# Kernel tuning notes

Measured on AMD Instinct MI355X. Metric: run time of the kernel, lower is better.

The kernel has to match this reference:

```python
import jax, jax.numpy as jnp
import numpy as np

B, N, K, H = 2, 2048, 48, 128
NIN = 2 * H          # num_in = 2*num_hidden (ProteinMPNN wiring)
FF = 4 * H           # PositionWiseFeedForward hidden
SCALE = 30.0
EPS = 1e-5           # torch LayerNorm default eps


def _ln(x, g, b):
    m = jnp.mean(x, axis=-1, keepdims=True)
    v = jnp.mean((x - m) ** 2, axis=-1, keepdims=True)
    return (x - m) / jnp.sqrt(v + EPS) * g + b


def _gelu(x):
    return jax.nn.gelu(x, approximate=False)  # torch.nn.GELU default (erf)


def _lin(x, W, b):
    return x @ W + b


def setup_inputs() -> dict:
    key = jax.random.key(0)
    ks = jax.random.split(key, 24)
    s = 0.05
    inp = {
        "h_V": jax.random.normal(ks[0], (B, N, H), jnp.float32),
        "h_E": jax.random.normal(ks[1], (B, N, K, H), jnp.float32),
        "E_idx": jax.random.randint(ks[2], (B, N, K), 0, N, jnp.int64),
        "mask_V": jnp.ones((B, N), jnp.float32),
        "mask_attend": jnp.ones((B, N, K), jnp.float32),
        # message MLP (node update): W1 in = H + NIN = 3H
        "W1": jax.random.normal(ks[3], (3 * H, H), jnp.float32) * s,
        "b1": jnp.zeros((H,), jnp.float32),
        "W2": jax.random.normal(ks[4], (H, H), jnp.float32) * s,
        "b2": jnp.zeros((H,), jnp.float32),
        "W3": jax.random.normal(ks[5], (H, H), jnp.float32) * s,
        "b3": jnp.zeros((H,), jnp.float32),
        # PositionWiseFeedForward
        "Wd_in": jax.random.normal(ks[6], (H, FF), jnp.float32) * s,
        "bd_in": jnp.zeros((FF,), jnp.float32),
        "Wd_out": jax.random.normal(ks[7], (FF, H), jnp.float32) * s,
        "bd_out": jnp.zeros((H,), jnp.float32),
        # edge-update MLP: W11 in = H + NIN = 3H
        "W11": jax.random.normal(ks[8], (3 * H, H), jnp.float32) * s,
        "b11": jnp.zeros((H,), jnp.float32),
        "W12": jax.random.normal(ks[9], (H, H), jnp.float32) * s,
        "b12": jnp.zeros((H,), jnp.float32),
        "W13": jax.random.normal(ks[10], (H, H), jnp.float32) * s,
        "b13": jnp.zeros((H,), jnp.float32),
        # LayerNorms
        "n1g": jnp.ones((H,), jnp.float32), "n1b": jnp.zeros((H,), jnp.float32),
        "n2g": jnp.ones((H,), jnp.float32), "n2b": jnp.zeros((H,), jnp.float32),
        "n3g": jnp.ones((H,), jnp.float32), "n3b": jnp.zeros((H,), jnp.float32),
    }
    return inp


def reference(h_V, h_E, E_idx, mask_V, mask_attend,
              W1, b1, W2, b2, W3, b3,
              Wd_in, bd_in, Wd_out, bd_out,
              W11, b11, W12, b12, W13, b13,
              n1g, n1b, n2g, n2b, n3g, n3b):
    gather = jax.vmap(lambda hv, idx: hv[idx])  # [B,N,H],[B,N,K] -> [B,N,K,H]

    # --- node update: cat_neighbors_nodes + expand + 3-layer GELU MLP ---
    h_nb = gather(h_V, E_idx)                                   # [B,N,K,H]
    hV_exp = jnp.broadcast_to(h_V[:, :, None, :], h_nb.shape)   # [B,N,K,H]
    h_EV = jnp.concatenate([hV_exp, h_E, h_nb], axis=-1)        # [B,N,K,3H]
    h_msg = _lin(_gelu(_lin(_gelu(_lin(h_EV, W1, b1)), W2, b2)), W3, b3)
    h_msg = mask_attend[..., None] * h_msg
    dh = jnp.sum(h_msg, axis=-2) / SCALE                        # masked-sum reduce
    h_V = _ln(h_V + dh, n1g, n1b)

    # --- position-wise FFN ---
    dh = _lin(_gelu(_lin(h_V, Wd_in, bd_in)), Wd_out, bd_out)
    h_V = _ln(h_V + dh, n2g, n2b)
    h_V = mask_V[..., None] * h_V

    # --- edge update (not last layer) ---
    h_nb2 = gather(h_V, E_idx)
    hV_exp2 = jnp.broadcast_to(h_V[:, :, None, :], h_nb2.shape)
    h_EV2 = jnp.concatenate([hV_exp2, h_E, h_nb2], axis=-1)     # [B,N,K,3H]
    h_msg2 = _lin(_gelu(_lin(_gelu(_lin(h_EV2, W11, b11)), W12, b12)), W13, b13)
    h_E = _ln(h_E + h_msg2, n3g, n3b)
    return (h_V, h_E)
```

## Files before the change

kernel.cpp:

```cpp
#include <hip/hip_runtime.h>
#include <stdint.h>

#define XP2 264
#define MP 136
#define EPIP 132
#define FFP 520

typedef __attribute__((ext_vector_type(8))) short bf16x8;
typedef __attribute__((ext_vector_type(4))) float f32x4;

__device__ __forceinline__ f32x4 mfma16(bf16x8 a, bf16x8 b, f32x4 c) {
  return __builtin_amdgcn_mfma_f32_16x16x32_bf16(a, b, c, 0, 0, 0);
}

__device__ __forceinline__ uint16_t f2b(float f) {
  union { float f; uint32_t u; } v; v.f = f;
  uint32_t u = v.u;
  uint32_t r = u + 0x7fffu + ((u >> 16) & 1u);
  return (uint16_t)(r >> 16);
}
__device__ __forceinline__ uint32_t pk2(float a, float b) {
  return (uint32_t)f2b(a) | ((uint32_t)f2b(b) << 16);
}
__device__ __forceinline__ float gelu_f(float x) {
  float z = 0.7978845608028654f * (x + 0.044715f * x * x * x);
  float e = __expf(2.0f * z);
  float t = 1.0f - 2.0f / (e + 1.0f);
  return 0.5f * x * (1.0f + t);
}

__global__ __launch_bounds__(256) void k_prep(
    const float* __restrict__ hV,
    const float* __restrict__ W1, const float* __restrict__ W2, const float* __restrict__ W3,
    const float* __restrict__ WdIn, const float* __restrict__ WdOut,
    const float* __restrict__ W11, const float* __restrict__ W12, const float* __restrict__ W13,
    uint16_t* __restrict__ hVb,
    uint16_t* __restrict__ W1t, uint16_t* __restrict__ W2t, uint16_t* __restrict__ W3t,
    uint16_t* __restrict__ WdInT, uint16_t* __restrict__ WdOutT,
    uint16_t* __restrict__ W11t, uint16_t* __restrict__ W12t, uint16_t* __restrict__ W13t) {
  int i = blockIdx.x * 256 + threadIdx.x;
  if (i < 524288) { hVb[i] = f2b(hV[i]); return; }
  int j = i - 524288;
  if (j < 49152) { int n = j / 384, k = j - n * 384; W1t[j] = f2b(W1[k * 128 + n]); return; }
  j -= 49152;
  if (j < 16384) { int n = j >> 7, k = j & 127; W2t[j] = f2b(W2[k * 128 + n]); return; }
  j -= 16384;
  if (j < 16384) { int n = j >> 7, k = j & 127; W3t[j] = f2b(W3[k * 128 + n]); return; }
  j -= 16384;
  if (j < 65536) { int n = j >> 7, k = j & 127; WdInT[j] = f2b(WdIn[k * 512 + n]); return; }
  j -= 65536;
  if (j < 65536) { int n = j >> 9, k = j & 511; WdOutT[j] = f2b(WdOut[k * 128 + n]); return; }
  j -= 65536;
  if (j < 49152) { int n = j / 384, k = j - n * 384; W11t[j] = f2b(W11[k * 128 + n]); return; }
  j -= 49152;
  if (j < 16384) { int n = j >> 7, k = j & 127; W12t[j] = f2b(W12[k * 128 + n]); return; }
  j -= 16384;
  if (j < 16384) { int n = j >> 7, k = j & 127; W13t[j] = f2b(W13[k * 128 + n]); return; }
}

__global__ __launch_bounds__(256) void k_vec(
    const uint16_t* __restrict__ Xb, const uint16_t* __restrict__ Wt,
    float* __restrict__ C) {
  const int tid = threadIdx.x;
  const int lane = tid & 63, w = tid >> 6, l15 = lane & 15, lg = lane >> 4;
  const int row0 = blockIdx.x * 64 + w * 16;
  f32x4 acc[8] = {};
#pragma unroll
  for (int ks = 0; ks < 4; ++ks) {
    bf16x8 a = *(const bf16x8*)(Xb + (row0 + l15) * 128 + ks * 32 + lg * 8);
#pragma unroll
    for (int j = 0; j < 8; ++j) {
      bf16x8 bb = *(const bf16x8*)(Wt + (j * 16 + l15) * 384 + ks * 32 + lg * 8);
      acc[j] = mfma16(a, bb, acc[j]);
    }
  }
#pragma unroll
  for (int j = 0; j < 8; ++j)
#pragma unroll
    for (int r = 0; r < 4; ++r)
      C[(row0 + lg * 4 + r) * 128 + j * 16 + l15] = acc[j][r];
}

#define BUILD_XT(GSRC)                                                              \
  do {                                                                              \
    for (int idx = tid; idx < 48 * 32; idx += 256) {                                \
      int k_ = idx >> 5;                                                            \
      int c_ = idx & 31;                                                            \
      uint4 v_;                                                                     \
      if (c_ < 16) {                                                                \
        const float* s_ = hE + (size_t)(bn * 48 + k_) * 128 + (c_ << 3);            \
        float4 f0_ = *(const float4*)s_;                                            \
        float4 f1_ = *(const float4*)(s_ + 4);                                      \
        v_ = make_uint4(pk2(f0_.x, f0_.y), pk2(f0_.z, f0_.w),                       \
                        pk2(f1_.x, f1_.y), pk2(f1_.z, f1_.w));                      \
      } else {                                                                      \
        v_ = *(const uint4*)((GSRC) + nbr[k_] * 128 + ((c_ - 16) << 3));            \
      }                                                                             \
      *(uint4*)(xt + k_ * XP2 + (c_ << 3)) = v_;                                    \
    }                                                                               \
  } while (0)

#define LAYER256(WT, ACC)                                                           \
  do {                                                                              \
    const uint16_t* wr0_ = (WT) + (w * 32 + l15) * 384 + 128 + lg * 8;              \
    const uint16_t* wr1_ = (WT) + (w * 32 + 16 + l15) * 384 + 128 + lg * 8;         \
    _Pragma("unroll 2") for (int ks = 0; ks < 8; ++ks) {                            \
      bf16x8 bA_ = *(const bf16x8*)(wr0_ + ks * 32);                                \
      bf16x8 bB_ = *(const bf16x8*)(wr1_ + ks * 32);                                \
      _Pragma("unroll") for (int m = 0; m < 3; ++m) {                               \
        bf16x8 a_ = *(const bf16x8*)(xt + (m * 16 + l15) * XP2 + ks * 32 + lg * 8); \
        ACC[m][0] = mfma16(a_, bA_, ACC[m][0]);                                     \
        ACC[m][1] = mfma16(a_, bB_, ACC[m][1]);                                     \
      }                                                                             \
    }                                                                               \
  } while (0)

#define LAYER128(WT, ASRC, ACC)                                                     \
  do {                                                                              \
    const uint16_t* wr0_ = (WT) + (w * 32 + l15) * 128 + lg * 8;                    \
    const uint16_t* wr1_ = (WT) + (w * 32 + 16 + l15) * 128 + lg * 8;               \
    _Pragma("unroll") for (int ks = 0; ks < 4; ++ks) {                              \
      bf16x8 bA_ = *(const bf16x8*)(wr0_ + ks * 32);                                \
      bf16x8 bB_ = *(const bf16x8*)(wr1_ + ks * 32);                                \
      _Pragma("unroll") for (int m = 0; m < 3; ++m) {                               \
        bf16x8 a_ = *(const bf16x8*)((ASRC) + (m * 16 + l15) * MP + ks * 32 + lg * 8); \
        ACC[m][0] = mfma16(a_, bA_, ACC[m][0]);                                     \
        ACC[m][1] = mfma16(a_, bB_, ACC[m][1]);                                     \
      }                                                                              \
    }                                                                               \
  } while (0)

#define GSTORE(ACC, BIAS, DST)                                                      \
  do {                                                                              \
    float bA_ = (BIAS)[w * 32 + l15];                                               \
    float bB_ = (BIAS)[w * 32 + 16 + l15];                                          \
    _Pragma("unroll") for (int m = 0; m < 3; ++m)                                   \
    _Pragma("unroll") for (int r = 0; r < 4; ++r) {                                 \
      int row_ = m * 16 + lg * 4 + r;                                               \
      (DST)[row_ * MP + w * 32 + l15] = f2b(gelu_f(ACC[m][0][r] + bA_));            \
      (DST)[row_ * MP + w * 32 + 16 + l15] = f2b(gelu_f(ACC[m][1][r] + bB_));       \
    }                                                                               \
  } while (0)

#define ACC_INIT(ACC, CV)                                                           \
  do {                                                                              \
    float c0_ = (CV)[bn * 128 + w * 32 + l15];                                      \
    float c1_ = (CV)[bn * 128 + w * 32 + 16 + l15];                                 \
    _Pragma("unroll") for (int m = 0; m < 3; ++m) {                                 \
      ACC[m][0] = (f32x4){c0_, c0_, c0_, c0_};                                      \
      ACC[m][1] = (f32x4){c1_, c1_, c1_, c1_};                                      \
    }                                                                               \
  } while (0)

__global__ __launch_bounds__(256, 4) void k_node(
    const float* __restrict__ hV, const float* __restrict__ hE,
    const int* __restrict__ eidx, const float* __restrict__ maskA,
    const float* __restrict__ bias1, const float* __restrict__ bias2,
    const float* __restrict__ bias3,
    const float* __restrict__ g1, const float* __restrict__ be1,
    const uint16_t* __restrict__ hVb, const float* __restrict__ C1,
    const uint16_t* __restrict__ W1t, const uint16_t* __restrict__ W2t,
    const uint16_t* __restrict__ W3t,
    float* __restrict__ hV1, uint16_t* __restrict__ hV1b) {
  __shared__ __align__(16) unsigned char lds[39296];
  uint16_t* xt = (uint16_t*)lds;
  uint16_t* midA = (uint16_t*)(lds + 25344);
  uint16_t* midB = (uint16_t*)lds;
  float* dh = (float*)(lds + 38400);
  int* nbr = (int*)(lds + 38912);
  float* amask = (float*)(lds + 39104);

  const int tid = threadIdx.x;
  const int lane = tid & 63;
  const int w = tid >> 6;
  const int l15 = lane & 15;
  const int lg = lane >> 4;
  const int bn = blockIdx.x;
  const int b = bn >> 11;

  if (tid < 48) {
    nbr[tid] = (b << 11) + eidx[bn * 48 + tid];
    amask[tid] = maskA[bn * 48 + tid];
  }
  __syncthreads();

  BUILD_XT(hVb);
  __syncthreads();

  f32x4 acc1[3][2];
  ACC_INIT(acc1, C1);
  LAYER256(W1t, acc1);
  GSTORE(acc1, bias1, midA);
  __syncthreads();

  f32x4 acc2[3][2] = {};
  LAYER128(W2t, midA, acc2);
  GSTORE(acc2, bias2, midB);
  __syncthreads();

  f32x4 acc3[3][2] = {};
  LAYER128(W3t, midB, acc3);

  {
    float bA = bias3[w * 32 + l15];
    float bB = bias3[w * 32 + 16 + l15];
    float s0 = 0.f, s1 = 0.f;
#pragma unroll
    for (int m = 0; m < 3; ++m)
#pragma unroll
      for (int r = 0; r < 4; ++r) {
        int row = m * 16 + lg * 4 + r;
        float mk = amask[row];
        s0 += (acc3[m][0][r] + bA) * mk;
        s1 += (acc3[m][1][r] + bB) * mk;
      }
    s0 += __shfl_xor(s0, 16); s0 += __shfl_xor(s0, 32);
    s1 += __shfl_xor(s1, 16); s1 += __shfl_xor(s1, 32);
    if (lg == 0) { dh[w * 32 + l15] = s0; dh[w * 32 + 16 + l15] = s1; }
  }
  __syncthreads();

  if (w == 0) {
    const float inv = 1.0f / 30.0f;
    float x0 = hV[bn * 128 + lane] + dh[lane] * inv;
    float x1 = hV[bn * 128 + 64 + lane] + dh[64 + lane] * inv;
    float s = x0 + x1, q = x0 * x0 + x1 * x1;
#pragma unroll
    for (int off = 1; off < 64; off <<= 1) {
      s += __shfl_xor(s, off);
      q += __shfl_xor(q, off);
    }
    float mean = s * (1.0f / 128.0f);
    float var = q * (1.0f / 128.0f) - mean * mean;
    float rstd = rsqrtf(var + 1e-5f);
    float y0 = (x0 - mean) * rstd * g1[lane] + be1[lane];
    float y1 = (x1 - mean) * rstd * g1[64 + lane] + be1[64 + lane];
    hV1[bn * 128 + lane] = y0;
    hV1[bn * 128 + 64 + lane] = y1;
    hV1b[bn * 128 + lane] = f2b(y0);
    hV1b[bn * 128 + 64 + lane] = f2b(y1);
  }
}

__global__ __launch_bounds__(256, 2) void k_ffn(
    const float* __restrict__ hV1, const uint16_t* __restrict__ hV1b,
    const float* __restrict__ maskV,
    const float* __restrict__ bdin, const float* __restrict__ bdout,
    const float* __restrict__ g2, const float* __restrict__ be2,
    const uint16_t* __restrict__ WdInT, const uint16_t* __restrict__ WdOutT,
    float* __restrict__ outV, uint16_t* __restrict__ hV2b) {
  __shared__ __align__(16) unsigned char lds[20992];
  uint16_t* xa = (uint16_t*)lds;
  uint16_t* mf = (uint16_t*)(lds + 4352);
  float* epi = (float*)(lds + 4352);

  const int tid = threadIdx.x;
  const int lane = tid & 63;
  const int w = tid >> 6;
  const int l15 = lane & 15;
  const int lg = lane >> 4;
  const int node0 = blockIdx.x * 16;

  {
    int row = tid >> 4, c = tid & 15;
    *(uint4*)(xa + row * 136 + (c << 3)) =
        *(const uint4*)(hV1b + (node0 + row) * 128 + (c << 3));
  }
  __syncthreads();

  f32x4 acc[8] = {};
  {
    const uint16_t* ar = xa + l15 * 136 + lg * 8;
#pragma unroll
    for (int ks = 0; ks < 4; ++ks) {
      bf16x8 a = *(const bf16x8*)(ar + ks * 32);
#pragma unroll
      for (int j = 0; j < 8; ++j) {
        bf16x8 bb = *(const bf16x8*)(WdInT + ((w * 8 + j) * 16 + l15) * 128 + ks * 32 + lg * 8);
        acc[j] = mfma16(a, bb, acc[j]);
      }
    }
  }
#pragma unroll
  for (int j = 0; j < 8; ++j) {
    int col = (w * 8 + j) * 16 + l15;
    float bs = bdin[col];
#pragma unroll
    for (int r = 0; r < 4; ++r) {
      int row = lg * 4 + r;
      mf[row * FFP + col] = f2b(gelu_f(acc[j][r] + bs));
    }
  }
  __syncthreads();

  f32x4 acc2[2] = {};
  {
    const uint16_t* mr = mf + l15 * FFP + lg * 8;
#pragma unroll 4
    for (int ks = 0; ks < 16; ++ks) {
      bf16x8 a = *(const bf16x8*)(mr + ks * 32);
#pragma unroll
      for (int t = 0; t < 2; ++t) {
        bf16x8 bb = *(const bf16x8*)(WdOutT + ((w * 2 + t) * 16 + l15) * 512 + ks * 32 + lg * 8);
        acc2[t] = mfma16(a, bb, acc2[t]);
      }
    }
  }
  __syncthreads();
#pragma unroll
  for (int t = 0; t < 2; ++t) {
    int col = (w * 2 + t) * 16 + l15;
    float bs = bdout[col];
#pragma unroll
    for (int r = 0; r < 4; ++r) {
      int row = lg * 4 + r;
      epi[row * EPIP + col] = acc2[t][r] + bs;
    }
  }
  __syncthreads();

#pragma unroll
  for (int rr = 0; rr < 4; ++rr) {
    int row = w * 4 + rr;
    int node = node0 + row;
    float x0 = epi[row * EPIP + lane] + hV1[node * 128 + lane];
    float x1 = epi[row * EPIP + 64 + lane] + hV1[node * 128 + 64 + lane];
    float s = x0 + x1, q = x0 * x0 + x1 * x1;
#pragma unroll
    for (int off = 1; off < 64; off <<= 1) {
      s += __shfl_xor(s, off);
      q += __shfl_xor(q, off);
    }
    float mean = s * (1.0f / 128.0f);
    float var = q * (1.0f / 128.0f) - mean * mean;
    float rstd = rsqrtf(var + 1e-5f);
    float mv = maskV[node];
    float y0 = mv * ((x0 - mean) * rstd * g2[lane] + be2[lane]);
    float y1 = mv * ((x1 - mean) * rstd * g2[64 + lane] + be2[64 + lane]);
    outV[node * 128 + lane] = y0;
    outV[node * 128 + 64 + lane] = y1;
    hV2b[node * 128 + lane] = f2b(y0);
    hV2b[node * 128 + 64 + lane] = f2b(y1);
  }
}

__global__ __launch_bounds__(256, 4) void k_edge(
    const float* __restrict__ hE, const int* __restrict__ eidx,
    const float* __restrict__ bias1, const float* __restrict__ bias2,
    const float* __restrict__ bias3,
    const float* __restrict__ g3, const float* __restrict__ be3,
    const uint16_t* __restrict__ hV2b, const float* __restrict__ C2,
    const uint16_t* __restrict__ W1t, const uint16_t* __restrict__ W2t,
    const uint16_t* __restrict__ W3t,
    float* __restrict__ outE) {
  __shared__ __align__(16) unsigned char lds[38592];
  uint16_t* xt = (uint16_t*)lds;
  uint16_t* midA = (uint16_t*)(lds + 25344);
  uint16_t* midB = (uint16_t*)lds;
  float* epi = (float*)lds;
  int* nbr = (int*)(lds + 38400);

  const int tid = threadIdx.x;
  const int lane = tid & 63;
  const int w = tid >> 6;
  const int l15 = lane & 15;
  const int lg = lane >> 4;
  const int bn = blockIdx.x;
  const int b = bn >> 11;

  if (tid < 48) nbr[tid] = (b << 11) + eidx[bn * 48 + tid];
  __syncthreads();

  BUILD_XT(hV2b);
  __syncthreads();

  f32x4 acc1[3][2];
  ACC_INIT(acc1, C2);
  LAYER256(W1t, acc1);
  GSTORE(acc1, bias1, midA);
  __syncthreads();

  f32x4 acc2[3][2] = {};
  LAYER128(W2t, midA, acc2);
  GSTORE(acc2, bias2, midB);
  __syncthreads();

  f32x4 acc3[3][2] = {};
  LAYER128(W3t, midB, acc3);
  __syncthreads();

  {
    float bA = bias3[w * 32 + l15];
    float bB = bias3[w * 32 + 16 + l15];
#pragma unroll
    for (int m = 0; m < 3; ++m)
#pragma unroll
      for (int r = 0; r < 4; ++r) {
        int row = m * 16 + lg * 4 + r;
        epi[row * EPIP + w * 32 + l15] = acc3[m][0][r] + bA;
        epi[row * EPIP + w * 32 + 16 + l15] = acc3[m][1][r] + bB;
      }
  }
  __syncthreads();

#pragma unroll
  for (int rr = 0; rr < 12; ++rr) {
    int row = w * 12 + rr;
    int e = bn * 48 + row;
    float x0 = epi[row * EPIP + lane] + hE[(size_t)e * 128 + lane];
    float x1 = epi[row * EPIP + 64 + lane] + hE[(size_t)e * 128 + 64 + lane];
    float s = x0 + x1, q = x0 * x0 + x1 * x1;
#pragma unroll
    for (int off = 1; off < 64; off <<= 1) {
      s += __shfl_xor(s, off);
      q += __shfl_xor(q, off);
    }
    float mean = s * (1.0f / 128.0f);
    float var = q * (1.0f / 128.0f) - mean * mean;
    float rstd = rsqrtf(var + 1e-5f);
    float y0 = (x0 - mean) * rstd * g3[lane] + be3[lane];
    float y1 = (x1 - mean) * rstd * g3[64 + lane] + be3[64 + lane];
    outE[(size_t)e * 128 + lane] = y0;
    outE[(size_t)e * 128 + 64 + lane] = y1;
  }
}

extern "C" void kernel_launch(void* const* d_in, const int* in_sizes, int n_in,
                              void* d_out, int out_size, void* d_ws, size_t ws_size,
                              hipStream_t stream) {
  const float* hV = (const float*)d_in[0];
  const float* hE = (const float*)d_in[1];
  const int* eidx = (const int*)d_in[2];
  const float* maskV = (const float*)d_in[3];
  const float* maskA = (const float*)d_in[4];
  const float* W1 = (const float*)d_in[5];   const float* b1 = (const float*)d_in[6];
  const float* W2 = (const float*)d_in[7];   const float* b2 = (const float*)d_in[8];
  const float* W3 = (const float*)d_in[9];   const float* b3 = (const float*)d_in[10];
  const float* WdIn = (const float*)d_in[11];  const float* bdin = (const float*)d_in[12];
  const float* WdOut = (const float*)d_in[13]; const float* bdout = (const float*)d_in[14];
  const float* W11 = (const float*)d_in[15]; const float* b11 = (const float*)d_in[16];
  const float* W12 = (const float*)d_in[17]; const float* b12 = (const float*)d_in[18];
  const float* W13 = (const float*)d_in[19]; const float* b13 = (const float*)d_in[20];
  const float* n1g = (const float*)d_in[21]; const float* n1b = (const float*)d_in[22];
  const float* n2g = (const float*)d_in[23]; const float* n2b = (const float*)d_in[24];
  const float* n3g = (const float*)d_in[25]; const float* n3b = (const float*)d_in[26];

  char* ws = (char*)d_ws;
  uint16_t* hVb    = (uint16_t*)(ws + 0);
  uint16_t* W1t    = (uint16_t*)(ws + 1048576);
  uint16_t* W2t    = (uint16_t*)(ws + 1146880);
  uint16_t* W3t    = (uint16_t*)(ws + 1179648);
  uint16_t* WdInT  = (uint16_t*)(ws + 1212416);
  uint16_t* WdOutT = (uint16_t*)(ws + 1343488);
  uint16_t* W11t   = (uint16_t*)(ws + 1474560);
  uint16_t* W12t   = (uint16_t*)(ws + 1572864);
  uint16_t* W13t   = (uint16_t*)(ws + 1605632);
  float*    hV1    = (float*)(ws + 1638400);
  uint16_t* hV1b   = (uint16_t*)(ws + 3735552);
  uint16_t* hV2b   = (uint16_t*)(ws + 4784128);
  float*    C1     = (float*)(ws + 5832704);
  float*    C2     = (float*)(ws + 7929856);

  float* outV = (float*)d_out;
  float* outE = (float*)d_out + 524288;

  k_prep<<<3200, 256, 0, stream>>>(hV, W1, W2, W3, WdIn, WdOut, W11, W12, W13,
                                   hVb, W1t, W2t, W3t, WdInT, WdOutT, W11t, W12t, W13t);
  k_vec<<<64, 256, 0, stream>>>(hVb, W1t, C1);
  k_node<<<4096, 256, 0, stream>>>(hV, hE, eidx, maskA, b1, b2, b3, n1g, n1b,
                                   hVb, C1, W1t, W2t, W3t, hV1, hV1b);
  k_ffn<<<256, 256, 0, stream>>>(hV1, hV1b, maskV, bdin, bdout, n2g, n2b,
                                 WdInT, WdOutT, outV, hV2b);
  k_vec<<<64, 256, 0, stream>>>(hV2b, W11t, C2);
  k_edge<<<4096, 256, 0, stream>>>(hE, eidx, b11, b12, b13, n3g, n3b,
                                   hV2b, C2, W11t, W12t, W13t, outE);
}
```

Before: 233.3 us.

## Feed first-layer MFMA operands directly from global memory and do LayerNorm in registers

```diff
diff --git a/kernel.cpp b/kernel.cpp
--- a/kernel.cpp
+++ b/kernel.cpp
@@ -1,7 +1,7 @@
 #include <hip/hip_runtime.h>
+#include <hip/hip_bf16.h>
 #include <stdint.h>
 
-#define XP2 264
 #define MP 136
 #define EPIP 132
 #define FFP 520
@@ -14,19 +14,19 @@
 }
 
 __device__ __forceinline__ uint16_t f2b(float f) {
-  union { float f; uint32_t u; } v; v.f = f;
-  uint32_t u = v.u;
-  uint32_t r = u + 0x7fffu + ((u >> 16) & 1u);
-  return (uint16_t)(r >> 16);
-}
-__device__ __forceinline__ uint32_t pk2(float a, float b) {
-  return (uint32_t)f2b(a) | ((uint32_t)f2b(b) << 16);
+  union { __hip_bfloat16 h; uint16_t u; } v;
+  v.h = __float2bfloat16(f);
+  return v.u;
+}
+__device__ __forceinline__ uint32_t pk2f(float a, float b) {
+  union { __hip_bfloat162 h; uint32_t u; } v;
+  v.h = __float22bfloat162_rn(make_float2(a, b));
+  return v.u;
 }
 __device__ __forceinline__ float gelu_f(float x) {
-  float z = 0.7978845608028654f * (x + 0.044715f * x * x * x);
-  float e = __expf(2.0f * z);
-  float t = 1.0f - 2.0f / (e + 1.0f);
-  return 0.5f * x * (1.0f + t);
+  float u = __builtin_fmaf(x * x, 0.044715f, 1.0f);
+  float e = __builtin_amdgcn_exp2f(-2.302585093f * x * u);
+  return x * __builtin_amdgcn_rcpf(1.0f + e);
 }
 
 __global__ __launch_bounds__(256) void k_prep(
@@ -81,34 +81,34 @@
       C[(row0 + lg * 4 + r) * 128 + j * 16 + l15] = acc[j][r];
 }
 
-#define BUILD_XT(GSRC)                                                              \
-  do {                                                                              \
-    for (int idx = tid; idx < 48 * 32; idx += 256) {                                \
-      int k_ = idx >> 5;                                                            \
-      int c_ = idx & 31;                                                            \
-      uint4 v_;                                                                     \
-      if (c_ < 16) {                                                                \
-        const float* s_ = hE + (size_t)(bn * 48 + k_) * 128 + (c_ << 3);            \
-        float4 f0_ = *(const float4*)s_;                                            \
-        float4 f1_ = *(const float4*)(s_ + 4);                                      \
-        v_ = make_uint4(pk2(f0_.x, f0_.y), pk2(f0_.z, f0_.w),                       \
-                        pk2(f1_.x, f1_.y), pk2(f1_.z, f1_.w));                      \
-      } else {                                                                      \
-        v_ = *(const uint4*)((GSRC) + nbr[k_] * 128 + ((c_ - 16) << 3));            \
-      }                                                                             \
-      *(uint4*)(xt + k_ * XP2 + (c_ << 3)) = v_;                                    \
-    }                                                                               \
-  } while (0)
-
-#define LAYER256(WT, ACC)                                                           \
+#define LAYER256G(WT, GSRC, ACC)                                                    \
   do {                                                                              \
     const uint16_t* wr0_ = (WT) + (w * 32 + l15) * 384 + 128 + lg * 8;              \
-    const uint16_t* wr1_ = (WT) + (w * 32 + 16 + l15) * 384 + 128 + lg * 8;         \
-    _Pragma("unroll 2") for (int ks = 0; ks < 8; ++ks) {                            \
+    const uint16_t* wr1_ = wr0_ + 16 * 384;                                         \
+    const float* heB_[3];                                                           \
+    const uint16_t* gvB_[3];                                                        \
+    _Pragma("unroll") for (int m = 0; m < 3; ++m) {                                 \
+      heB_[m] = hE + (size_t)(bn * 48 + m * 16 + l15) * 128 + lg * 8;               \
+      gvB_[m] = (GSRC) + (size_t)nbr[m * 16 + l15] * 128 + lg * 8;                  \
+    }                                                                               \
+    _Pragma("unroll") for (int ks = 0; ks < 4; ++ks) {                              \
       bf16x8 bA_ = *(const bf16x8*)(wr0_ + ks * 32);                                \
       bf16x8 bB_ = *(const bf16x8*)(wr1_ + ks * 32);                                \
       _Pragma("unroll") for (int m = 0; m < 3; ++m) {                               \
-        bf16x8 a_ = *(const bf16x8*)(xt + (m * 16 + l15) * XP2 + ks * 32 + lg * 8); \
+        float4 f0_ = *(const float4*)(heB_[m] + ks * 32);                           \
+        float4 f1_ = *(const float4*)(heB_[m] + ks * 32 + 4);                       \
+        union { bf16x8 v; uint32_t u[4]; } a_;                                      \
+        a_.u[0] = pk2f(f0_.x, f0_.y); a_.u[1] = pk2f(f0_.z, f0_.w);                 \
+        a_.u[2] = pk2f(f1_.x, f1_.y); a_.u[3] = pk2f(f1_.z, f1_.w);                 \
+        ACC[m][0] = mfma16(a_.v, bA_, ACC[m][0]);                                   \
+        ACC[m][1] = mfma16(a_.v, bB_, ACC[m][1]);                                   \
+      }                                                                             \
+    }                                                                               \
+    _Pragma("unroll") for (int ks = 4; ks < 8; ++ks) {                              \
+      bf16x8 bA_ = *(const bf16x8*)(wr0_ + ks * 32);                                \
+      bf16x8 bB_ = *(const bf16x8*)(wr1_ + ks * 32);                                \
+      _Pragma("unroll") for (int m = 0; m < 3; ++m) {                               \
+        bf16x8 a_ = *(const bf16x8*)(gvB_[m] + (ks - 4) * 32);                      \
         ACC[m][0] = mfma16(a_, bA_, ACC[m][0]);                                     \
         ACC[m][1] = mfma16(a_, bB_, ACC[m][1]);                                     \
       }                                                                             \
@@ -118,7 +118,7 @@
 #define LAYER128(WT, ASRC, ACC)                                                     \
   do {                                                                              \
     const uint16_t* wr0_ = (WT) + (w * 32 + l15) * 128 + lg * 8;                    \
-    const uint16_t* wr1_ = (WT) + (w * 32 + 16 + l15) * 128 + lg * 8;               \
+    const uint16_t* wr1_ = wr0_ + 16 * 128;                                         \
     _Pragma("unroll") for (int ks = 0; ks < 4; ++ks) {                              \
       bf16x8 bA_ = *(const bf16x8*)(wr0_ + ks * 32);                                \
       bf16x8 bB_ = *(const bf16x8*)(wr1_ + ks * 32);                                \
@@ -152,7 +152,7 @@
     }                                                                               \
   } while (0)
 
-__global__ __launch_bounds__(256, 4) void k_node(
+__global__ __launch_bounds__(256, 6) void k_node(
     const float* __restrict__ hV, const float* __restrict__ hE,
     const int* __restrict__ eidx, const float* __restrict__ maskA,
     const float* __restrict__ bias1, const float* __restrict__ bias2,
@@ -162,13 +162,11 @@
     const uint16_t* __restrict__ W1t, const uint16_t* __restrict__ W2t,
     const uint16_t* __restrict__ W3t,
     float* __restrict__ hV1, uint16_t* __restrict__ hV1b) {
-  __shared__ __align__(16) unsigned char lds[39296];
-  uint16_t* xt = (uint16_t*)lds;
-  uint16_t* midA = (uint16_t*)(lds + 25344);
-  uint16_t* midB = (uint16_t*)lds;
-  float* dh = (float*)(lds + 38400);
-  int* nbr = (int*)(lds + 38912);
-  float* amask = (float*)(lds + 39104);
+  __shared__ __align__(16) unsigned char lds[26624];
+  uint16_t* midA = (uint16_t*)lds;
+  uint16_t* midB = (uint16_t*)(lds + 13056);
+  int* nbr = (int*)(lds + 26112);
+  float* dh = (float*)(lds + 26112);
 
   const int tid = threadIdx.x;
   const int lane = tid & 63;
@@ -178,18 +176,12 @@
   const int bn = blockIdx.x;
   const int b = bn >> 11;
 
-  if (tid < 48) {
-    nbr[tid] = (b << 11) + eidx[bn * 48 + tid];
-    amask[tid] = maskA[bn * 48 + tid];
-  }
-  __syncthreads();
-
-  BUILD_XT(hVb);
+  if (tid < 48) nbr[tid] = (b << 11) + eidx[bn * 48 + tid];
   __syncthreads();
 
   f32x4 acc1[3][2];
   ACC_INIT(acc1, C1);
-  LAYER256(W1t, acc1);
+  LAYER256G(W1t, hVb, acc1);
   GSTORE(acc1, bias1, midA);
   __syncthreads();
 
@@ -210,7 +202,7 @@
 #pragma unroll
       for (int r = 0; r < 4; ++r) {
         int row = m * 16 + lg * 4 + r;
-        float mk = amask[row];
+        float mk = maskA[bn * 48 + row];
         s0 += (acc3[m][0][r] + bA) * mk;
         s1 += (acc3[m][1][r] + bB) * mk;
       }
@@ -344,7 +336,7 @@
   }
 }
 
-__global__ __launch_bounds__(256, 4) void k_edge(
+__global__ __launch_bounds__(256, 6) void k_edge(
     const float* __restrict__ hE, const int* __restrict__ eidx,
     const float* __restrict__ bias1, const float* __restrict__ bias2,
     const float* __restrict__ bias3,
@@ -353,12 +345,13 @@
     const uint16_t* __restrict__ W1t, const uint16_t* __restrict__ W2t,
     const uint16_t* __restrict__ W3t,
     float* __restrict__ outE) {
-  __shared__ __align__(16) unsigned char lds[38592];
-  uint16_t* xt = (uint16_t*)lds;
-  uint16_t* midA = (uint16_t*)(lds + 25344);
-  uint16_t* midB = (uint16_t*)lds;
-  float* epi = (float*)lds;
-  int* nbr = (int*)(lds + 38400);
+  __shared__ __align__(16) unsigned char lds[26304];
+  uint16_t* midA = (uint16_t*)lds;
+  uint16_t* midB = (uint16_t*)(lds + 13056);
+  int* nbr = (int*)(lds + 26112);
+  float* part_s = (float*)lds;
+  float* part_q = (float*)(lds + 768);
+  float* mstd = (float*)(lds + 1536);
 
   const int tid = threadIdx.x;
   const int lane = tid & 63;
@@ -371,12 +364,9 @@
   if (tid < 48) nbr[tid] = (b << 11) + eidx[bn * 48 + tid];
   __syncthreads();
 
-  BUILD_XT(hV2b);
-  __syncthreads();
-
   f32x4 acc1[3][2];
   ACC_INIT(acc1, C2);
-  LAYER256(W1t, acc1);
+  LAYER256G(W1t, hV2b, acc1);
   GSTORE(acc1, bias1, midA);
   __syncthreads();
 
@@ -387,42 +377,53 @@
 
   f32x4 acc3[3][2] = {};
   LAYER128(W3t, midB, acc3);
-  __syncthreads();
-
-  {
-    float bA = bias3[w * 32 + l15];
-    float bB = bias3[w * 32 + 16 + l15];
-#pragma unroll
-    for (int m = 0; m < 3; ++m)
-#pragma unroll
-      for (int r = 0; r < 4; ++r) {
-        int row = m * 16 + lg * 4 + r;
-        epi[row * EPIP + w * 32 + l15] = acc3[m][0][r] + bA;
-        epi[row * EPIP + w * 32 + 16 + l15] = acc3[m][1][r] + bB;
-      }
-  }
-  __syncthreads();
-
-#pragma unroll
-  for (int rr = 0; rr < 12; ++rr) {
-    int row = w * 12 + rr;
-    int e = bn * 48 + row;
-    float x0 = epi[row * EPIP + lane] + hE[(size_t)e * 128 + lane];
-    float x1 = epi[row * EPIP + 64 + lane] + hE[(size_t)e * 128 + 64 + lane];
-    float s = x0 + x1, q = x0 * x0 + x1 * x1;
-#pragma unroll
-    for (int off = 1; off < 64; off <<= 1) {
-      s += __shfl_xor(s, off);
-      q += __shfl_xor(q, off);
-    }
+
+  const float bA = bias3[w * 32 + l15];
+  const float bB = bias3[w * 32 + 16 + l15];
+
+#pragma unroll
+  for (int m = 0; m < 3; ++m)
+#pragma unroll
+    for (int r = 0; r < 4; ++r) {
+      int row = m * 16 + lg * 4 + r;
+      size_t e = (size_t)bn * 48 + row;
+      float x0 = acc3[m][0][r] + bA + hE[e * 128 + w * 32 + l15];
+      float x1 = acc3[m][1][r] + bB + hE[e * 128 + w * 32 + 16 + l15];
+      float s = x0 + x1;
+      float q = x0 * x0 + x1 * x1;
+      s += __shfl_xor(s, 1); q += __shfl_xor(q, 1);
+      s += __shfl_xor(s, 2); q += __shfl_xor(q, 2);
+      s += __shfl_xor(s, 4); q += __shfl_xor(q, 4);
+      s += __shfl_xor(s, 8); q += __shfl_xor(q, 8);
+      if (l15 == 0) { part_s[row * 4 + w] = s; part_q[row * 4 + w] = q; }
+    }
+  __syncthreads();
+
+  if (tid < 48) {
+    float s = part_s[tid * 4] + part_s[tid * 4 + 1] + part_s[tid * 4 + 2] + part_s[tid * 4 + 3];
+    float q = part_q[tid * 4] + part_q[tid * 4 + 1] + part_q[tid * 4 + 2] + part_q[tid * 4 + 3];
     float mean = s * (1.0f / 128.0f);
     float var = q * (1.0f / 128.0f) - mean * mean;
-    float rstd = rsqrtf(var + 1e-5f);
-    float y0 = (x0 - mean) * rstd * g3[lane] + be3[lane];
-    float y1 = (x1 - mean) * rstd * g3[64 + lane] + be3[64 + lane];
-    outE[(size_t)e * 128 + lane] = y0;
-    outE[(size_t)e * 128 + 64 + lane] = y1;
-  }
+    mstd[tid * 2] = mean;
+    mstd[tid * 2 + 1] = rsqrtf(var + 1e-5f);
+  }
+  __syncthreads();
+
+  const float gA = g3[w * 32 + l15], beA = be3[w * 32 + l15];
+  const float gB = g3[w * 32 + 16 + l15], beB = be3[w * 32 + 16 + l15];
+#pragma unroll
+  for (int m = 0; m < 3; ++m)
+#pragma unroll
+    for (int r = 0; r < 4; ++r) {
+      int row = m * 16 + lg * 4 + r;
+      size_t e = (size_t)bn * 48 + row;
+      float mean = mstd[row * 2];
+      float rstd = mstd[row * 2 + 1];
+      float x0 = acc3[m][0][r] + bA + hE[e * 128 + w * 32 + l15];
+      float x1 = acc3[m][1][r] + bB + hE[e * 128 + w * 32 + 16 + l15];
+      outE[e * 128 + w * 32 + l15] = (x0 - mean) * rstd * gA + beA;
+      outE[e * 128 + w * 32 + 16 + l15] = (x1 - mean) * rstd * gB + beB;
+    }
 }
 
 extern "C" void kernel_launch(void* const* d_in, const int* in_sizes, int n_in,
```

New measurement: 308.1 us. 32.1% more time.
